# Kernel optimization log

Measured on AMD Instinct MI355X. Metric: run time of the kernel, lower is better.

## Reference

```python
import jax, jax.numpy as jnp
import numpy as np

K = 3
P = 14
INV_SQRT2 = 0.7071067811865476  # db1 (Haar) filter coefficient
EPS = 1e-4


def _pool(x):
    # adaptive_avg_pool2d to (P, P); H, W divisible by P -> uniform mean pooling
    N, C, H, W = x.shape
    return x.reshape(N, C, P, H // P, P, W // P).mean(axis=(3, 5))


def setup_inputs() -> dict:
    key = jax.random.key(0)
    ks = jax.random.split(key, 8)
    N, C, H, W = 64, 3, 224, 224
    D, Cin = 540, 30  # D_clip=D_hidden=540, n_bands*3 = 30
    return {
        "frames": jax.random.normal(ks[0], (N, C, H, W), jnp.float32),
        "t_clip": jax.random.normal(ks[1], (N, D, P, P), jnp.float32),
        "w1": jax.random.normal(ks[2], (D, Cin), jnp.float32) * 0.05,
        "b1": jnp.zeros((D,), jnp.float32),
        "w2": jax.random.normal(ks[3], (D, D), jnp.float32) * 0.05,
        "b2": jnp.zeros((D,), jnp.float32),
        "wg": jax.random.normal(ks[4], (D, 2 * D, 3, 3), jnp.float32) * 0.05,
        "bg": jnp.zeros((D,), jnp.float32),
    }


def reference(frames, t_clip, w1, b1, w2, b2, wg, bg):
    # Batched Haar SWT2 (a trous, periodic), levels 1..K, fully vectorized over
    # (N, C) -- replaces the per-frame/per-channel pywt.swt2 CPU loop.
    a = frames
    bands = []  # per level: HL (cH), LH (cV), HH (cD), each (N, C, H, W)
    for j in range(K):
        d = 2 ** j  # filter dilation at level j+1
        lx = (a + jnp.roll(a, -d, axis=-1)) * INV_SQRT2
        hx = (a - jnp.roll(a, -d, axis=-1)) * INV_SQRT2
        cA = (lx + jnp.roll(lx, -d, axis=-2)) * INV_SQRT2
        cH = (lx - jnp.roll(lx, -d, axis=-2)) * INV_SQRT2
        cV = (hx + jnp.roll(hx, -d, axis=-2)) * INV_SQRT2
        cD = (hx - jnp.roll(hx, -d, axis=-2)) * INV_SQRT2
        bands += [cH, cV, cD]
        a = cA
    # per-(frame, channel) 99th-percentile normalization + pool to (P, P)
    pooled = []
    for b in bands:
        s = jnp.quantile(jnp.abs(b), 0.99, axis=(-2, -1), keepdims=True)
        pooled.append(_pool(b / (s + EPS)))
    # LL band (level K approximation): mean-center then quantile-scale
    mu = a.mean(axis=(-2, -1), keepdims=True)
    s = jnp.quantile(jnp.abs(a - mu), 0.99, axis=(-2, -1), keepdims=True)
    pooled.append(_pool((a - mu) / (s + EPS)))
    e_pix = jnp.concatenate(pooled, axis=1)  # (N, 30, P, P)

    # 1x1 conv -> relu -> 1x1 conv -> tanh
    h = jax.nn.relu(jnp.einsum("ncpq,dc->ndpq", e_pix, w1) + b1[None, :, None, None])
    m = jnp.tanh(jnp.einsum("ncpq,dc->ndpq", h, w2) + b2[None, :, None, None])

    # gated fusion with CLIP patch tokens
    gi = jnp.concatenate([t_clip, m], axis=1)  # (N, 2*D, P, P)
    g = jax.lax.conv_general_dilated(
        gi, wg, (1, 1), "SAME", dimension_numbers=("NCHW", "OIHW", "NCHW")
    ) + bg[None, :, None, None]
    gamma = jax.nn.sigmoid(g)
    return t_clip + gamma * m
```

## Files before the change

### kernel.cpp

```cpp
#include <hip/hip_runtime.h>

typedef unsigned short u16;
typedef unsigned int u32;
typedef __bf16 bf16x8 __attribute__((ext_vector_type(8)));
typedef float f32x4 __attribute__((ext_vector_type(4)));

constexpr int NB = 64, CH3 = 3;
constexpr int PLANES = NB * CH3;
constexpr int PPIX = 224 * 224;
constexpr int PP = 196;
constexpr int NPX = NB * PP;
constexpr int K2 = 576;
constexpr int CIPAD = 1088;
constexpr int KCONV = 9 * CIPAD;
constexpr int BINS = 256;
constexpr int BIN0 = 896;
constexpr int RANK1 = 49674;
constexpr int RANK2 = 49675;

constexpr size_t OFF_HIST = 0;
constexpr size_t SZ_HIST  = (size_t)10 * PLANES * BINS * 4;
constexpr size_t OFF_SUMS = OFF_HIST + SZ_HIST;
constexpr size_t OFF_INVS = OFF_SUMS + 768;
constexpr size_t OFF_BSUM = OFF_INVS + 7680;
constexpr size_t SZ_BSUM  = (size_t)10 * PLANES * PP * 4;
constexpr size_t OFF_EPIX = OFF_BSUM + SZ_BSUM;
constexpr size_t OFF_HBF  = OFF_EPIX + (size_t)NPX * 32 * 4;
constexpr size_t OFF_GIT  = OFF_HBF + (size_t)NPX * K2 * 2;
constexpr size_t SZ_GIT   = (size_t)NB * 256 * CIPAD * 2;
constexpr size_t OFF_WGB  = OFF_GIT + SZ_GIT;
constexpr size_t OFF_W2B  = OFF_WGB + (size_t)640 * KCONV * 2;
constexpr size_t OFF_MARR = OFF_W2B + (size_t)640 * K2 * 2;

__device__ __forceinline__ u16 f2bf(float x) {
  union { float f; u32 u; } c; c.f = x;
  u32 r = c.u + 0x7FFFu + ((c.u >> 16) & 1u);
  return (u16)(r >> 16);
}

__device__ __forceinline__ float wred64(float v) {
  v += __shfl_down(v, 32, 64); v += __shfl_down(v, 16, 64);
  v += __shfl_down(v, 8, 64);  v += __shfl_down(v, 4, 64);
  v += __shfl_down(v, 2, 64);  v += __shfl_down(v, 1, 64);
  return v;
}

__device__ __forceinline__ float gred16(float v) {
  v += __shfl_down(v, 8, 16); v += __shfl_down(v, 4, 16);
  v += __shfl_down(v, 2, 16); v += __shfl_down(v, 1, 16);
  return v;
}

__device__ __forceinline__ int hbin(float v) {
  int b = (int)(__float_as_uint(fabsf(v)) >> 20) - BIN0;
  return min(max(b, 0), BINS - 1);
}

__device__ __forceinline__ void cp16(const void* g, void* l) {
  __builtin_amdgcn_global_load_lds((const __attribute__((address_space(1))) u32*)g,
                                   (__attribute__((address_space(3))) u32*)l, 16, 0, 0);
}

#define BAR_MEM() asm volatile("s_barrier" ::: "memory")

constexpr int RSTRIDE = 10 * 128 + 8;
__global__ __launch_bounds__(256) void swt_fused_kernel(const float* __restrict__ frames,
    float* __restrict__ sums, int* __restrict__ hist, float* __restrict__ bsum)
{
  __shared__ float f0[23 * 224];
  __shared__ float a1[22 * 224];
  __shared__ float a2[20 * 224];
  __shared__ u32 lh[4 * RSTRIDE];
  __shared__ float csum[14 * 10];
  __shared__ float wsum[4];
  const int t = threadIdx.x;
  const int rb = blockIdx.x, plane = blockIdx.y;
  const float* Pp = frames + (size_t)plane * PPIX;

  for (int i = t; i < 23 * 224; i += 256) {
    int r = i / 224, c = i - r * 224;
    int gr = rb * 16 + r; if (gr >= 224) gr -= 224;
    f0[i] = Pp[gr * 224 + c];
  }
  for (int i = t; i < 4 * RSTRIDE; i += 256) lh[i] = 0;
  __syncthreads();

  u32* lhr = &lh[(t & 3) * RSTRIDE];
  const int cell0 = (t >> 4) * 10;
  float ps = 0.f;

  if (t < 224) {
    int c2 = t + 1; if (c2 >= 224) c2 -= 224;
    float sH = 0.f, sV = 0.f, sD = 0.f;
    for (int r = 0; r < 22; ++r) {
      float p00 = f0[r * 224 + t], p01 = f0[r * 224 + c2];
      float p10 = f0[(r + 1) * 224 + t], p11 = f0[(r + 1) * 224 + c2];
      float sa = p00 + p01, sb = p10 + p11, da = p00 - p01, db = p10 - p11;
      a1[r * 224 + t] = (sa + sb) * 0.5f;
      if (r < 16) {
        float cH = (sa - sb) * 0.5f, cV = (da + db) * 0.5f, cD = (da - db) * 0.5f;
        int bH = hbin(cH), bV = hbin(cV), bD = hbin(cD);
        atomicAdd(&lhr[0 * 128 + (bH >> 1)], 1u << ((bH & 1) * 16));
        atomicAdd(&lhr[1 * 128 + (bV >> 1)], 1u << ((bV & 1) * 16));
        atomicAdd(&lhr[2 * 128 + (bD >> 1)], 1u << ((bD & 1) * 16));
        sH += cH; sV += cV; sD += cD;
        ps += p00;
      }
    }
    sH = gred16(sH); sV = gred16(sV); sD = gred16(sD);
    if ((t & 15) == 0) { csum[cell0 + 0] = sH; csum[cell0 + 1] = sV; csum[cell0 + 2] = sD; }
  }
  ps = wred64(ps);
  if ((t & 63) == 0) wsum[t >> 6] = ps;
  __syncthreads();
  if (t == 0) atomicAdd(&sums[plane], wsum[0] + wsum[1] + wsum[2] + wsum[3]);

  if (t < 224) {
    int c2 = t + 2; if (c2 >= 224) c2 -= 224;
    float sH = 0.f, sV = 0.f, sD = 0.f;
    for (int r = 0; r < 20; ++r) {
      float p00 = a1[r * 224 + t], p01 = a1[r * 224 + c2];
      float p10 = a1[(r + 2) * 224 + t], p11 = a1[(r + 2) * 224 + c2];
      float sa = p00 + p01, sb = p10 + p11, da = p00 - p01, db = p10 - p11;
      a2[r * 224 + t] = (sa + sb) * 0.5f;
      if (r < 16) {
        float cH = (sa - sb) * 0.5f, cV = (da + db) * 0.5f, cD = (da - db) * 0.5f;
        int bH = hbin(cH), bV = hbin(cV), bD = hbin(cD);
        atomicAdd(&lhr[3 * 128 + (bH >> 1)], 1u << ((bH & 1) * 16));
        atomicAdd(&lhr[4 * 128 + (bV >> 1)], 1u << ((bV & 1) * 16));
        atomicAdd(&lhr[5 * 128 + (bD >> 1)], 1u << ((bD & 1) * 16));
        sH += cH; sV += cV; sD += cD;
      }
    }
    sH = gred16(sH); sV = gred16(sV); sD = gred16(sD);
    if ((t & 15) == 0) { csum[cell0 + 3] = sH; csum[cell0 + 4] = sV; csum[cell0 + 5] = sD; }
  }
  __syncthreads();

  if (t < 224) {
    int c2 = t + 4; if (c2 >= 224) c2 -= 224;
    float sH = 0.f, sV = 0.f, sD = 0.f, sA = 0.f;
    for (int r = 0; r < 16; ++r) {
      float p00 = a2[r * 224 + t], p01 = a2[r * 224 + c2];
      float p10 = a2[(r + 4) * 224 + t], p11 = a2[(r + 4) * 224 + c2];
      float sa = p00 + p01, sb = p10 + p11, da = p00 - p01, db = p10 - p11;
      float cA = (sa + sb) * 0.5f;
      float cH = (sa - sb) * 0.5f, cV = (da + db) * 0.5f, cD = (da - db) * 0.5f;
      int bH = hbin(cH), bV = hbin(cV), bD = hbin(cD), bA = hbin(cA);
      atomicAdd(&lhr[6 * 128 + (bH >> 1)], 1u << ((bH & 1) * 16));
      atomicAdd(&lhr[7 * 128 + (bV >> 1)], 1u << ((bV & 1) * 16));
      atomicAdd(&lhr[8 * 128 + (bD >> 1)], 1u << ((bD & 1) * 16));
      atomicAdd(&lhr[9 * 128 + (bA >> 1)], 1u << ((bA & 1) * 16));
      sH += cH; sV += cV; sD += cD; sA += cA;
    }
    sH = gred16(sH); sV = gred16(sV); sD = gred16(sD); sA = gred16(sA);
    if ((t & 15) == 0) {
      csum[cell0 + 6] = sH; csum[cell0 + 7] = sV; csum[cell0 + 8] = sD; csum[cell0 + 9] = sA;
    }
  }
  __syncthreads();

  for (int i = t; i < 10 * 256; i += 256) {
    int bg = i >> 8, b = i & 255;
    u32 acc = 0;
#pragma unroll
    for (int rp = 0; rp < 4; ++rp)
      acc += (lh[rp * RSTRIDE + bg * 128 + (b >> 1)] >> ((b & 1) * 16)) & 0xFFFFu;
    if (acc) atomicAdd(&hist[((size_t)bg * PLANES + plane) * BINS + b], (int)acc);
  }
  if (t < 140) {
    int cell = t / 10, bg = t - cell * 10;
    bsum[((size_t)bg * PLANES + plane) * PP + rb * 14 + cell] = csum[cell * 10 + bg];
  }
}

__global__ __launch_bounds__(256) void quant_kernel(const int* __restrict__ hist,
    float* __restrict__ invs)
{
  const int g = blockIdx.x;
  __shared__ int h[BINS];
  const int t = threadIdx.x;
  h[t] = hist[(size_t)g * BINS + t];
  __syncthreads();
  if (t == 0) {
    float v[2] = {0.f, 0.f};
    int cum = 0, target = 0;
    for (int b = 0; b < BINS && target < 2; ++b) {
      int c = h[b];
      while (target < 2) {
        int rank = target ? RANK2 : RANK1;
        if (cum + c >= rank) {
          float lo = __uint_as_float((u32)(b + BIN0) << 20);
          float hi = __uint_as_float((u32)(b + BIN0 + 1) << 20);
          float fr = ((float)(rank - cum) - 0.5f) / (float)c;
          fr = fminf(fmaxf(fr, 0.f), 1.f);
          v[target] = lo + (hi - lo) * fr;
          ++target;
        } else break;
      }
      cum += c;
    }
    float s = 0.75f * v[0] + 0.25f * v[1];
    invs[g] = 1.f / (s + 1e-4f);
  }
}

__global__ __launch_bounds__(256) void epix_kernel(const float* __restrict__ bsum,
    const float* __restrict__ sums, const float* __restrict__ invs, float* __restrict__ epix)
{
  int tid = blockIdx.x * 256 + threadIdx.x;
  int ch = tid & 31, px = tid >> 5;
  int n = px / PP, q = px - n * PP;
  float val = 0.f;
  if (ch < 27) {
    int bg = ch / 3, c = ch - bg * 3;
    int plane = n * 3 + c;
    val = bsum[((size_t)bg * PLANES + plane) * PP + q] * (1.f / 256.f) * invs[bg * PLANES + plane];
  } else if (ch < 30) {
    int c = ch - 27, plane = n * 3 + c;
    float mu = sums[plane] * (8.f / 50176.f);
    val = (bsum[((size_t)9 * PLANES + plane) * PP + q] * (1.f / 256.f) - mu) * invs[9 * PLANES + plane];
  }
  epix[tid] = val;
}

__global__ __launch_bounds__(256) void pack_wg_kernel(const float* __restrict__ wg,
    u16* __restrict__ wgb)
{
  __shared__ float w[9720];
  const int oc = blockIdx.x;
  const int t = threadIdx.x;
  if (oc < 540) {
    for (int i = t; i < 9720; i += 256) w[i] = wg[(size_t)oc * 9720 + i];
  }
  __syncthreads();
  for (int j = t; j < KCONV; j += 256) {
    int kc = j >> 6, i = j & 63;
    int cib = kc / 9, tap = kc - cib * 9;
    int ci = cib * 64 + i;
    float v = (oc < 540 && ci < 1080) ? w[ci * 9 + tap] : 0.f;
    wgb[(size_t)oc * KCONV + j] = f2bf(v);
  }
}

__global__ __launch_bounds__(256) void pack_w2_kernel(const float* __restrict__ w2,
    u16* __restrict__ w2b)
{
  int tid = blockIdx.x * 256 + threadIdx.x;
  int oc = tid / K2, cc = tid - oc * K2;
  float v = (oc < 540 && cc < 540) ? w2[oc * 540 + cc] : 0.f;
  w2b[tid] = f2bf(v);
}

__global__ __launch_bounds__(256) void fill_git_kernel(const float* __restrict__ tclip,
    u16* __restrict__ git)
{
  __shared__ float tile[64][65];
  const int n = blockIdx.z, ct = blockIdx.y, qt = blockIdx.x;
  const int t = threadIdx.x, tr = t >> 6, tc = t & 63;
#pragma unroll 4
  for (int i = 0; i < 16; ++i) {
    int ci = ct * 64 + i * 4 + tr, q = qt * 64 + tc;
    float v = (ci < 540 && q < 196) ? tclip[((size_t)n * 540 + ci) * 196 + q] : 0.f;
    tile[i * 4 + tr][tc] = v;
  }
  __syncthreads();
#pragma unroll 4
  for (int i = 0; i < 16; ++i) {
    int q = qt * 64 + i * 4 + tr, ci = ct * 64 + tc;
    if (q < 196 && ci < 540) {
      int y = q / 14, x = q - y * 14;
      git[(((size_t)n * 16 + 1 + y) * 16 + 1 + x) * CIPAD + ci] = f2bf(tile[tc][i * 4 + tr]);
    }
  }
}

__global__ __launch_bounds__(256) void gemm1_kernel(const float* __restrict__ epix,
    const float* __restrict__ w1, const float* __restrict__ b1, u16* __restrict__ hbf)
{
  __shared__ float es[64][33];
  __shared__ float w1s[128][33];
  const int t = threadIdx.x;
  const int px0 = blockIdx.x * 64, oc0 = blockIdx.y * 128;
  for (int i = t; i < 64 * 32; i += 256) { int r = i >> 5, cc = i & 31; es[r][cc] = epix[(size_t)(px0 + r) * 32 + cc]; }
  for (int i = t; i < 128 * 32; i += 256) {
    int r = i >> 5, cc = i & 31; int oc = oc0 + r;
    w1s[r][cc] = (oc < 540 && cc < 30) ? w1[oc * 30 + cc] : 0.f;
  }
  __syncthreads();
  const int ocl = t & 31, pxl = (t >> 5) * 8;
  float acc[4][8];
#pragma unroll
  for (int i = 0; i < 4; ++i)
#pragma unroll
    for (int j = 0; j < 8; ++j) acc[i][j] = 0.f;
  for (int k = 0; k < 30; ++k) {
    float wv[4], ev[8];
#pragma unroll
    for (int i = 0; i < 4; ++i) wv[i] = w1s[ocl + 32 * i][k];
#pragma unroll
    for (int j = 0; j < 8; ++j) ev[j] = es[pxl + j][k];
#pragma unroll
    for (int i = 0; i < 4; ++i)
#pragma unroll
      for (int j = 0; j < 8; ++j) acc[i][j] += wv[i] * ev[j];
  }
#pragma unroll
  for (int i = 0; i < 4; ++i) {
    int oc = oc0 + ocl + 32 * i;
    if (oc >= 576) continue;
    float bv = (oc < 540) ? b1[oc] : 0.f;
#pragma unroll
    for (int j = 0; j < 8; ++j) {
      int px = px0 + pxl + j;
      float v = (oc < 540) ? fmaxf(acc[i][j] + bv, 0.f) : 0.f;
      hbf[(size_t)px * K2 + oc] = f2bf(v);
    }
  }
}

template <int MODE>
__global__ __launch_bounds__(256) void mfma_gemm_kernel(
    const u16* __restrict__ A, const u16* __restrict__ Bm,
    const float* __restrict__ bias,
    float* __restrict__ marr, u16* __restrict__ git,
    const float* __restrict__ tclip, float* __restrict__ outp)
{
  constexpr int KCPB = (MODE == 1) ? 153 : 9;
  constexpr int BSTRIDE = (MODE == 1) ? KCONV : K2;
  __shared__ u16 smem[32768];
  const int t = threadIdx.x;
  const int lane = t & 63, wave = t >> 6;
  const int wm = wave & 1, wn = wave >> 1;

  int px0, oc0;
  if constexpr (MODE == 1) {
    int orig = blockIdx.x;
    int xcd = orig & 7, off = orig >> 3;
    constexpr int q = 61, r = 2;
    int wg = (xcd < r ? xcd * (q + 1) : r * (q + 1) + (xcd - r) * q) + off;
    int bx = wg / 5, by = wg - bx * 5;
    px0 = bx * 128; oc0 = by * 128;
  } else {
    px0 = blockIdx.x * 128; oc0 = blockIdx.y * 128;
  }

  const u16* aSrc[4];
  const u16* bSrc[4];
  int dstOff[4];
#pragma unroll
  for (int r = 0; r < 4; ++r) {
    int slot = r * 256 + t;
    int row = slot >> 3;
    int gs = ((slot ^ row) & 7) << 3;
    if constexpr (MODE == 0) {
      aSrc[r] = A + (size_t)(px0 + row) * K2 + gs;
    } else {
      int px = px0 + row;
      int n = px / 196, q2 = px - n * 196;
      int y = q2 / 14, x = q2 - y * 14;
      aSrc[r] = A + (size_t)((n * 16 + y) * 16 + x) * CIPAD + gs;
    }
    bSrc[r] = Bm + (size_t)(oc0 + row) * BSTRIDE + gs;
    dstOff[r] = (r * 256 + wave * 64) * 8;
  }

  auto stage = [&](int kcg, int buf) {
    int boff = kcg * 64;
    int aoff;
    if constexpr (MODE == 1) {
      int cib = kcg / 9, tap = kcg - cib * 9;
      int ky = tap / 3, kx = tap - ky * 3;
      aoff = (ky * 16 + kx) * CIPAD + cib * 64;
    } else aoff = boff;
    u16* As = smem + buf * 16384;
    u16* Bs = As + 8192;
#pragma unroll
    for (int r = 0; r < 4; ++r) cp16(aSrc[r] + aoff, As + dstOff[r]);
#pragma unroll
    for (int r = 0; r < 4; ++r) cp16(bSrc[r] + boff, Bs + dstOff[r]);
  };

  const int tx = lane & 15, quad = lane >> 4, l7 = lane & 7;
  int rowA[4], rowB[4];
#pragma unroll
  for (int i = 0; i < 4; ++i) {
    rowA[i] = (wm * 64 + i * 16 + tx) * 64;
    rowB[i] = (wn * 64 + i * 16 + tx) * 64;
  }

  f32x4 acc[4][4];
#pragma unroll
  for (int i = 0; i < 4; ++i)
#pragma unroll
    for (int j = 0; j < 4; ++j) acc[i][j] = (f32x4){0.f, 0.f, 0.f, 0.f};

  stage(0, 0);
  stage(1, 1);
  int cur = 0;
  for (int kc = 0; kc < KCPB; ++kc) {
    if (kc + 1 < KCPB) { asm volatile("s_waitcnt vmcnt(8)" ::: "memory"); }
    else               { asm volatile("s_waitcnt vmcnt(0)" ::: "memory"); }
    BAR_MEM();
    const u16* As = smem + cur * 16384;
    const u16* Bs = As + 8192;
#pragma unroll
    for (int ks = 0; ks < 2; ++ks) {
      int goff = (((ks * 4 + quad) ^ l7) << 3);
      bf16x8 af[4], bfr[4];
#pragma unroll
      for (int i = 0; i < 4; ++i) af[i] = *reinterpret_cast<const bf16x8*>(As + rowA[i] + goff);
#pragma unroll
      for (int i = 0; i < 4; ++i) bfr[i] = *reinterpret_cast<const bf16x8*>(Bs + rowB[i] + goff);
      __builtin_amdgcn_s_setprio(1);
#pragma unroll
      for (int i = 0; i < 4; ++i)
#pragma unroll
        for (int j = 0; j < 4; ++j)
          acc[i][j] = __builtin_amdgcn_mfma_f32_16x16x32_bf16(af[i], bfr[j], acc[i][j], 0, 0, 0);
      __builtin_amdgcn_s_setprio(0);
    }
    BAR_MEM();
    if (kc + 2 < KCPB) stage(kc + 2, cur);
    cur ^= 1;
  }

#pragma unroll
  for (int j = 0; j < 4; ++j) {
    int oc = oc0 + wn * 64 + j * 16 + tx;
    if (oc >= 540) continue;
    float bv = bias[oc];
#pragma unroll
    for (int i = 0; i < 4; ++i) {
      f32x4 v = acc[i][j];
      int px = px0 + wm * 64 + i * 16 + quad * 4;
      int n = px / 196, q2 = px - n * 196;
      size_t idx = ((size_t)(n * 540 + oc)) * 196 + q2;
      if constexpr (MODE == 0) {
#pragma unroll
        for (int r = 0; r < 4; ++r) {
          float val = tanhf(v[r] + bv);
          marr[idx + r] = val;
          int qq = q2 + r;
          int y = qq / 14, x = qq - y * 14;
          git[((n * 16 + 1 + y) * 16 + 1 + x) * CIPAD + 540 + oc] = f2bf(val);
        }
      } else {
        f32x4 mv = *reinterpret_cast<const f32x4*>(marr + idx);
        f32x4 tv = *reinterpret_cast<const f32x4*>(tclip + idx);
        f32x4 res;
#pragma unroll
        for (int r = 0; r < 4; ++r) {
          float g = v[r] + bv;
          res[r] = tv[r] + mv[r] / (1.f + expf(-g));
        }
        *reinterpret_cast<f32x4*>(outp + idx) = res;
      }
    }
  }
}

extern "C" void kernel_launch(void* const* d_in, const int* in_sizes, int n_in,
                              void* d_out, int out_size, void* d_ws, size_t ws_size,
                              hipStream_t stream)
{
  const float* frames = (const float*)d_in[0];
  const float* t_clip = (const float*)d_in[1];
  const float* w1 = (const float*)d_in[2];
  const float* b1 = (const float*)d_in[3];
  const float* w2 = (const float*)d_in[4];
  const float* b2 = (const float*)d_in[5];
  const float* wg = (const float*)d_in[6];
  const float* bg = (const float*)d_in[7];
  float* out = (float*)d_out;
  char* ws = (char*)d_ws;

  int* HIST = (int*)(ws + OFF_HIST);
  float* SUMS = (float*)(ws + OFF_SUMS);
  float* INVS = (float*)(ws + OFF_INVS);
  float* BSUM = (float*)(ws + OFF_BSUM);
  float* EPIX = (float*)(ws + OFF_EPIX);
  u16* HBF = (u16*)(ws + OFF_HBF);
  u16* GIT = (u16*)(ws + OFF_GIT);
  u16* WGB = (u16*)(ws + OFF_WGB);
  u16* W2B = (u16*)(ws + OFF_W2B);
  float* MARR = (float*)(ws + OFF_MARR);

  hipMemsetAsync(ws + OFF_HIST, 0, SZ_HIST + 768, stream);
  hipMemsetAsync(ws + OFF_GIT, 0, SZ_GIT, stream);

  pack_wg_kernel<<<640, 256, 0, stream>>>(wg, WGB);
  pack_w2_kernel<<<1440, 256, 0, stream>>>(w2, W2B);
  fill_git_kernel<<<dim3(4, 9, 64), 256, 0, stream>>>(t_clip, GIT);

  swt_fused_kernel<<<dim3(14, PLANES), 256, 0, stream>>>(frames, SUMS, HIST, BSUM);
  quant_kernel<<<1920, 256, 0, stream>>>(HIST, INVS);
  epix_kernel<<<1568, 256, 0, stream>>>(BSUM, SUMS, INVS, EPIX);

  gemm1_kernel<<<dim3(196, 5), 256, 0, stream>>>(EPIX, w1, b1, HBF);
  mfma_gemm_kernel<0><<<dim3(98, 5), 256, 0, stream>>>(HBF, W2B, b2, MARR, GIT, nullptr, nullptr);
  mfma_gemm_kernel<1><<<490, 256, 0, stream>>>(GIT, WGB, bg, MARR, nullptr, t_clip, out);
}
```

Measured before the change: 480.6 us.

## Stream SWT input from global, parallelize quantile scan, zero only GIT halo

Several independent changes land together. The SWT kernel drops its shared f0 staging buffer and reads frame rows straight from global memory with a rolling register window, and it doubles the LDS histogram replicas from 4 to 8 to cut atomic contention. The quantile kernel replaces its serial single-thread bin walk with a parallel prefix scan across 256 threads. The full memset of the padded GIT buffer is replaced by a kernel that zeroes only the halo border and the padding channel chunk, which assumes fill_git writes every interior element.

Result: no change. 484.5 us (+0.8%).

```diff
diff --git a/kernel.cpp b/kernel.cpp
--- a/kernel.cpp
+++ b/kernel.cpp
@@ -67,35 +67,31 @@
 __global__ __launch_bounds__(256) void swt_fused_kernel(const float* __restrict__ frames,
     float* __restrict__ sums, int* __restrict__ hist, float* __restrict__ bsum)
 {
-  __shared__ float f0[23 * 224];
   __shared__ float a1[22 * 224];
   __shared__ float a2[20 * 224];
-  __shared__ u32 lh[4 * RSTRIDE];
+  __shared__ u32 lh[8 * RSTRIDE];
   __shared__ float csum[14 * 10];
   __shared__ float wsum[4];
   const int t = threadIdx.x;
   const int rb = blockIdx.x, plane = blockIdx.y;
   const float* Pp = frames + (size_t)plane * PPIX;
 
-  for (int i = t; i < 23 * 224; i += 256) {
-    int r = i / 224, c = i - r * 224;
-    int gr = rb * 16 + r; if (gr >= 224) gr -= 224;
-    f0[i] = Pp[gr * 224 + c];
-  }
-  for (int i = t; i < 4 * RSTRIDE; i += 256) lh[i] = 0;
-  __syncthreads();
-
-  u32* lhr = &lh[(t & 3) * RSTRIDE];
+  for (int i = t; i < 8 * RSTRIDE; i += 256) lh[i] = 0;
+  __syncthreads();
+
+  u32* lhr = &lh[(t & 7) * RSTRIDE];
   const int cell0 = (t >> 4) * 10;
   float ps = 0.f;
 
   if (t < 224) {
     int c2 = t + 1; if (c2 >= 224) c2 -= 224;
     float sH = 0.f, sV = 0.f, sD = 0.f;
+    int gr0 = rb * 16; if (gr0 >= 224) gr0 -= 224;
+    float q00 = Pp[gr0 * 224 + t], q01 = Pp[gr0 * 224 + c2];
     for (int r = 0; r < 22; ++r) {
-      float p00 = f0[r * 224 + t], p01 = f0[r * 224 + c2];
-      float p10 = f0[(r + 1) * 224 + t], p11 = f0[(r + 1) * 224 + c2];
-      float sa = p00 + p01, sb = p10 + p11, da = p00 - p01, db = p10 - p11;
+      int gr1 = rb * 16 + r + 1; if (gr1 >= 224) gr1 -= 224;
+      float p10 = Pp[gr1 * 224 + t], p11 = Pp[gr1 * 224 + c2];
+      float sa = q00 + q01, sb = p10 + p11, da = q00 - q01, db = p10 - p11;
       a1[r * 224 + t] = (sa + sb) * 0.5f;
       if (r < 16) {
         float cH = (sa - sb) * 0.5f, cV = (da + db) * 0.5f, cD = (da - db) * 0.5f;
@@ -104,8 +100,9 @@
         atomicAdd(&lhr[1 * 128 + (bV >> 1)], 1u << ((bV & 1) * 16));
         atomicAdd(&lhr[2 * 128 + (bD >> 1)], 1u << ((bD & 1) * 16));
         sH += cH; sV += cV; sD += cD;
-        ps += p00;
+        ps += q00;
       }
+      q00 = p10; q01 = p11;
     }
     sH = gred16(sH); sV = gred16(sV); sD = gred16(sD);
     if ((t & 15) == 0) { csum[cell0 + 0] = sH; csum[cell0 + 1] = sV; csum[cell0 + 2] = sD; }
@@ -164,7 +161,7 @@
     int bg = i >> 8, b = i & 255;
     u32 acc = 0;
 #pragma unroll
-    for (int rp = 0; rp < 4; ++rp)
+    for (int rp = 0; rp < 8; ++rp)
       acc += (lh[rp * RSTRIDE + bg * 128 + (b >> 1)] >> ((b & 1) * 16)) & 0xFFFFu;
     if (acc) atomicAdd(&hist[((size_t)bg * PLANES + plane) * BINS + b], (int)acc);
   }
@@ -178,29 +175,33 @@
     float* __restrict__ invs)
 {
   const int g = blockIdx.x;
-  __shared__ int h[BINS];
+  __shared__ int cum[BINS];
+  __shared__ float vv[2];
   const int t = threadIdx.x;
-  h[t] = hist[(size_t)g * BINS + t];
+  const int c = hist[(size_t)g * BINS + t];
+  cum[t] = c;
+  __syncthreads();
+  for (int off = 1; off < BINS; off <<= 1) {
+    int y = (t >= off) ? cum[t - off] : 0;
+    __syncthreads();
+    cum[t] += y;
+    __syncthreads();
+  }
+  int inc = cum[t], prev = inc - c;
+#pragma unroll
+  for (int k = 0; k < 2; ++k) {
+    int rank = k ? RANK2 : RANK1;
+    if (prev < rank && rank <= inc) {
+      float lo = __uint_as_float((u32)(t + BIN0) << 20);
+      float hi = __uint_as_float((u32)(t + BIN0 + 1) << 20);
+      float fr = ((float)(rank - prev) - 0.5f) / (float)c;
+      fr = fminf(fmaxf(fr, 0.f), 1.f);
+      vv[k] = lo + (hi - lo) * fr;
+    }
+  }
   __syncthreads();
   if (t == 0) {
-    float v[2] = {0.f, 0.f};
-    int cum = 0, target = 0;
-    for (int b = 0; b < BINS && target < 2; ++b) {
-      int c = h[b];
-      while (target < 2) {
-        int rank = target ? RANK2 : RANK1;
-        if (cum + c >= rank) {
-          float lo = __uint_as_float((u32)(b + BIN0) << 20);
-          float hi = __uint_as_float((u32)(b + BIN0 + 1) << 20);
-          float fr = ((float)(rank - cum) - 0.5f) / (float)c;
-          fr = fminf(fmaxf(fr, 0.f), 1.f);
-          v[target] = lo + (hi - lo) * fr;
-          ++target;
-        } else break;
-      }
-      cum += c;
-    }
-    float s = 0.75f * v[0] + 0.25f * v[1];
+    float s = 0.75f * vv[0] + 0.25f * vv[1];
     invs[g] = 1.f / (s + 1e-4f);
   }
 }
@@ -224,6 +225,27 @@
   epix[tid] = val;
 }
 
+__global__ __launch_bounds__(256) void zero_halo_kernel(u16* __restrict__ git)
+{
+  constexpr int CPB = 136;
+  constexpr int CPN = 60 * CPB + 196;
+  int tid = blockIdx.x * 256 + threadIdx.x;
+  if (tid >= NB * CPN) return;
+  int n = tid / CPN, rem = tid - n * CPN;
+  int y, x, c;
+  if (rem < 60 * CPB) {
+    int bi = rem / CPB; c = rem - bi * CPB;
+    if (bi < 16) { y = 0; x = bi; }
+    else if (bi < 32) { y = 15; x = bi - 16; }
+    else { int i = bi - 32; y = 1 + (i >> 1); x = (i & 1) * 15; }
+  } else {
+    int q = rem - 60 * CPB;
+    y = 1 + q / 14; x = 1 + q % 14; c = 135;
+  }
+  f32x4 z = (f32x4){0.f, 0.f, 0.f, 0.f};
+  *reinterpret_cast<f32x4*>(&git[((size_t)(n * 256 + y * 16 + x)) * CIPAD + c * 8]) = z;
+}
+
 __global__ __launch_bounds__(256) void pack_wg_kernel(const float* __restrict__ wg,
     u16* __restrict__ wgb)
 {
@@ -487,8 +509,8 @@
   float* MARR = (float*)(ws + OFF_MARR);
 
   hipMemsetAsync(ws + OFF_HIST, 0, SZ_HIST + 768, stream);
-  hipMemsetAsync(ws + OFF_GIT, 0, SZ_GIT, stream);
-
+
+  zero_halo_kernel<<<(NB * (60 * 136 + 196) + 255) / 256, 256, 0, stream>>>(GIT);
   pack_wg_kernel<<<640, 256, 0, stream>>>(wg, WGB);
   pack_w2_kernel<<<1440, 256, 0, stream>>>(w2, W2B);
   fill_git_kernel<<<dim3(4, 9, 64), 256, 0, stream>>>(t_clip, GIT);
```
